# Kernel tuning notes

Hardware: AMD Instinct MI355X
Metric: run time of the kernel (lower is better)

Reference implementation:

```python
import jax, jax.numpy as jnp
import numpy as np

BOS, PAD, EOS, UNK = 0, 1, 2, 3  # fairseq dictionary special-token ids
CHAR_VOCAB = 5000
DIM = 512
LATENT = 10000


def setup_inputs() -> dict:
    key = jax.random.key(0)
    k1, k2, k3 = jax.random.split(key, 3)
    # char-ngram ids per token: [B, T, max_char_len]
    x = jax.random.randint(k1, (8, 1024, 20), 0, CHAR_VOCAB, dtype=jnp.int64 if jax.config.jax_enable_x64 else jnp.int32)
    # char ngram embedding table (also serves as preset_emb for special tokens)
    char_table = jax.random.normal(k2, (CHAR_VOCAB, DIM), dtype=jnp.float32) * 0.05
    # fixed latent codebook, init std = latent**-0.5 as in the module
    latent_mat = jax.random.normal(k3, (LATENT, DIM), dtype=jnp.float32) * (LATENT ** -0.5)
    return {"x": x, "char_table": char_table, "latent_mat": latent_mat}


def reference(x, char_table, latent_mat):
    # --- CharacterNgramEmbedder: gather + sum-pool over char ngrams (pad masked) ---
    emb = char_table[x]                                   # [B, T, C, D]
    valid = (x != PAD)[..., None].astype(emb.dtype)       # pad ngrams contribute 0
    ngram_weight = jnp.sum(emb * valid, axis=2)           # [B, T, D]
    lang_emb = jnp.tanh(ngram_weight)

    # --- latent codebook attention: QK^T -> softmax -> V over fixed codebook ---
    latent_scores = jnp.einsum('btd,ld->btl', lang_emb, latent_mat)   # [B, T, L]
    latent_dist = jax.nn.softmax(latent_scores, axis=-1)
    latent_emb = jnp.einsum('btl,ld->btd', latent_dist, latent_mat)   # [B, T, D]
    sde_emb = lang_emb + latent_emb

    # --- preset_emb overwrite for special tokens (masked scatter) ---
    first = x[:, :, 0]                                    # [B, T]
    for tok in (PAD, BOS, EOS, UNK):
        sde_emb = jnp.where((first == tok)[..., None], char_table[tok], sde_emb)
    return sde_emb
```

## Files before the change

### kernel.cpp

```cpp
#include <hip/hip_runtime.h>

#define BT    8192
#define DIM   512
#define NLAT  10000
#define LPAD2 10240
#define NG    20
#define CV    5000

typedef short bf16x8 __attribute__((ext_vector_type(8)));
typedef float f32x4  __attribute__((ext_vector_type(4)));
typedef unsigned short u16;
typedef u16 u16x8 __attribute__((ext_vector_type(8)));
typedef u16 u16x4 __attribute__((ext_vector_type(4)));

static __device__ __forceinline__ u16 f2bf(float f) {
    union { float f; unsigned u; } v; v.f = f;
    unsigned r = v.u + 0x7FFF + ((v.u >> 16) & 1);
    return (u16)(r >> 16);
}
static __device__ __forceinline__ float bf2f(u16 b) {
    union { unsigned u; float f; } v; v.u = ((unsigned)b) << 16; return v.f;
}

static __device__ __forceinline__ void gload16(const void* g, void* l) {
    __builtin_amdgcn_global_load_lds(
        (const __attribute__((address_space(1))) unsigned int*)g,
        (__attribute__((address_space(3))) unsigned int*)l,
        16, 0, 0);
}

__global__ __launch_bounds__(256) void ct2bf_kernel(
        const float* __restrict__ ct, u16* __restrict__ ctb) {
    const long base = ((long)blockIdx.x * 256 + threadIdx.x) * 8;
    float4 a = *(const float4*)(ct + base);
    float4 b = *(const float4*)(ct + base + 4);
    u16x8 v = { f2bf(a.x), f2bf(a.y), f2bf(a.z), f2bf(a.w),
                f2bf(b.x), f2bf(b.y), f2bf(b.z), f2bf(b.w) };
    *(u16x8*)(ctb + base) = v;
}

__global__ __launch_bounds__(256) void lang_kernel(
        const int* __restrict__ x, const u16* __restrict__ ctb,
        float* __restrict__ lang, u16* __restrict__ qb) {
    const int tok = blockIdx.x * 4 + (threadIdx.x >> 6);
    const int tl  = threadIdx.x & 63;
    const int* xr = x + tok * NG;
    float s[8];
    #pragma unroll
    for (int i = 0; i < 8; ++i) s[i] = 0.f;
    #pragma unroll
    for (int j = 0; j < NG; ++j) {
        int c = xr[j];
        if (c != 1) {
            u16x8 v = *(const u16x8*)(ctb + (long)c * DIM + tl * 8);
            #pragma unroll
            for (int i = 0; i < 8; ++i) s[i] += bf2f(v[i]);
        }
    }
    float4 lo, hi;
    lo.x = tanhf(s[0]); lo.y = tanhf(s[1]); lo.z = tanhf(s[2]); lo.w = tanhf(s[3]);
    hi.x = tanhf(s[4]); hi.y = tanhf(s[5]); hi.z = tanhf(s[6]); hi.w = tanhf(s[7]);
    *(float4*)(lang + (long)tok * DIM + tl * 8)     = lo;
    *(float4*)(lang + (long)tok * DIM + tl * 8 + 4) = hi;
    u16x8 o = { f2bf(lo.x), f2bf(lo.y), f2bf(lo.z), f2bf(lo.w),
                f2bf(hi.x), f2bf(hi.y), f2bf(hi.z), f2bf(hi.w) };
    *(u16x8*)(qb + (long)tok * DIM + tl * 8) = o;
}

__global__ __launch_bounds__(256) void conv_kernel(
        const float* __restrict__ lm, u16* __restrict__ kvg, u16* __restrict__ latT) {
    __shared__ u16 tile[64][514];
    const int lb = blockIdx.x * 64;
    const int t  = threadIdx.x;

    #pragma unroll 4
    for (int i = 0; i < 16; ++i) {
        int ch  = t + i * 256;
        int r   = ch >> 6;
        int c8  = ch & 63;
        int row = lb + r;
        u16x8 v = {0,0,0,0,0,0,0,0};
        if (row < NLAT) {
            const float* src = lm + (long)row * DIM + c8 * 8;
            float4 a = *(const float4*)src;
            float4 b = *(const float4*)(src + 4);
            v[0]=f2bf(a.x); v[1]=f2bf(a.y); v[2]=f2bf(a.z); v[3]=f2bf(a.w);
            v[4]=f2bf(b.x); v[5]=f2bf(b.y); v[6]=f2bf(b.z); v[7]=f2bf(b.w);
        }
        *(u16x8*)(kvg + (long)row * DIM + c8 * 8) = v;
        #pragma unroll
        for (int j = 0; j < 8; ++j) tile[r][c8 * 8 + j] = v[j];
    }
    __syncthreads();
    #pragma unroll 4
    for (int i = 0; i < 16; ++i) {
        int ch = t + i * 256;
        int d  = ch >> 3;
        int c8 = ch & 7;
        u16x8 v;
        #pragma unroll
        for (int j = 0; j < 8; ++j) v[j] = tile[c8 * 8 + j][d];
        *(u16x8*)(latT + (long)d * LPAD2 + lb + c8 * 8) = v;
    }
}

#define G_COMPUTE(buf) {                                                       \
    _Pragma("unroll")                                                          \
    for (int kc_ = 0; kc_ < 2; ++kc_) {                                        \
        const int xs_ = ((kc_ * 4 + g) ^ (lr & 7)) * 8;                        \
        bf16x8 af_[2], bf_[4];                                                 \
        _Pragma("unroll")                                                      \
        for (int mf_ = 0; mf_ < 2; ++mf_)                                      \
            af_[mf_] = *(const bf16x8*)&lds[buf][(wm * 32 + mf_ * 16 + lr) * 64 + xs_]; \
        _Pragma("unroll")                                                      \
        for (int nf_ = 0; nf_ < 4; ++nf_)                                      \
            bf_[nf_] = *(const bf16x8*)&lds[buf][8192 + (wn * 64 + nf_ * 16 + lr) * 64 + xs_]; \
        __builtin_amdgcn_s_setprio(1);                                         \
        _Pragma("unroll")                                                      \
        for (int mf_ = 0; mf_ < 2; ++mf_)                                      \
            _Pragma("unroll")                                                  \
            for (int nf_ = 0; nf_ < 4; ++nf_)                                  \
                acc[mf_][nf_] = __builtin_amdgcn_mfma_f32_16x16x32_bf16(       \
                    af_[mf_], bf_[nf_], acc[mf_][nf_], 0, 0, 0);               \
        __builtin_amdgcn_s_setprio(0);                                         \
    }                                                                          \
}

#define G1_STAGE(buf, kt) {                                                    \
    const int k0_ = (kt) * 64;                                                 \
    _Pragma("unroll")                                                          \
    for (int i_ = 0; i_ < 2; ++i_) {                                           \
        int ch_ = t + i_ * 512;                                                \
        int row_ = ch_ >> 3;                                                   \
        int sc_ = ((ch_ & 7) ^ (row_ & 7)) * 8;                                \
        gload16(Q + (m0 + row_) * (long)DIM + k0_ + sc_, &lds[buf][ch_ * 8]);  \
        gload16(Bgp + (long)row_ * DIM + k0_ + sc_, &lds[buf][8192 + ch_ * 8]);\
    }                                                                          \
}

__global__ __launch_bounds__(512, 4) void gemm1_kernel(
        const u16* __restrict__ Q, const u16* __restrict__ L,
        u16* __restrict__ P, float* __restrict__ rowsum,
        int n0_global, int npanels, int pstride) {
    __shared__ u16 lds[2][16384];

    const int nwg = 64 * npanels;
    const int cpx = nwg >> 3;
    const int bid = blockIdx.x;
    const int wg  = (bid & 7) * cpx + (bid >> 3);
    const int mb  = wg & 63;
    const int nb  = wg >> 6;
    const long m0    = (long)mb * 128;
    const int  ncol0 = n0_global + nb * 128;

    const u16* Bgp = L + (long)ncol0 * DIM;

    const int t = threadIdx.x, lane = t & 63, w = t >> 6;
    const int wm = w >> 1, wn = w & 1;
    const int g = lane >> 4, lr = lane & 15;

    f32x4 acc[2][4];
    #pragma unroll
    for (int m = 0; m < 2; ++m)
        #pragma unroll
        for (int n = 0; n < 4; ++n) acc[m][n] = f32x4{0.f,0.f,0.f,0.f};

    G1_STAGE(0, 0);
    G1_STAGE(1, 1);

    #pragma unroll 1
    for (int kt = 0; kt < 7; ++kt) {
        asm volatile("s_waitcnt vmcnt(4)" ::: "memory");
        __builtin_amdgcn_s_barrier();
        G_COMPUTE(kt & 1);
        __builtin_amdgcn_s_barrier();
        if (kt + 2 < 8) G1_STAGE(kt & 1, kt + 2);
    }
    asm volatile("s_waitcnt vmcnt(0)" ::: "memory");
    __builtin_amdgcn_s_barrier();
    G_COMPUTE(1);

    #pragma unroll
    for (int mf = 0; mf < 2; ++mf)
        #pragma unroll
        for (int nf = 0; nf < 4; ++nf) {
            const int col = ncol0 + wn * 64 + nf * 16 + lr;
            const bool ok = (col < NLAT);
            const int lcol = wn * 64 + nf * 16 + lr;
            #pragma unroll
            for (int r = 0; r < 4; ++r) {
                float p = ok ? __expf(acc[mf][nf][r]) : 0.f;
                acc[mf][nf][r] = p;
                const int row = wm * 32 + mf * 16 + g * 4 + r;
                lds[0][row * 128 + (lcol ^ ((row & 15) << 3))] = f2bf(p);
            }
        }

    #pragma unroll
    for (int mf = 0; mf < 2; ++mf) {
        float sv[4] = {0.f, 0.f, 0.f, 0.f};
        #pragma unroll
        for (int nf = 0; nf < 4; ++nf)
            #pragma unroll
            for (int r = 0; r < 4; ++r) sv[r] += acc[mf][nf][r];
        #pragma unroll
        for (int r = 0; r < 4; ++r) {
            float s = sv[r];
            s += __shfl_xor(s, 1); s += __shfl_xor(s, 2);
            s += __shfl_xor(s, 4); s += __shfl_xor(s, 8);
            if (lr == 0)
                atomicAdd(&rowsum[m0 + wm * 32 + mf * 16 + g * 4 + r], s);
        }
    }

    __syncthreads();
    const int pbase = ncol0 - n0_global;
    #pragma unroll
    for (int it = 0; it < 4; ++it) {
        const int flat = t + it * 512;
        const int row = flat >> 4, ck = flat & 15;
        u16x8 v = *(const u16x8*)&lds[0][row * 128 + ((ck ^ (row & 15)) * 8)];
        *(u16x8*)(P + (m0 + row) * (long)pstride + pbase + ck * 8) = v;
    }
}

#define G2_STAGE(buf, kt) {                                                    \
    const int kloc_ = (step_off + (kt)) * 64;                                  \
    _Pragma("unroll")                                                          \
    for (int i_ = 0; i_ < 2; ++i_) {                                           \
        int ch_ = t + i_ * 512;                                                \
        int row_ = ch_ >> 3;                                                   \
        int sc_ = ((ch_ & 7) ^ (row_ & 7)) * 8;                                \
        gload16(P + (m0 + row_) * (long)pstride + kloc_ + sc_, &lds[buf][ch_ * 8]); \
        gload16(LT + (long)(nbase + row_) * LPAD2 + n0_global + kloc_ + sc_,   \
                &lds[buf][8192 + ch_ * 8]);                                    \
    }                                                                          \
}

__global__ __launch_bounds__(512, 4) void gemm2_kernel(
        const u16* __restrict__ P, const u16* __restrict__ LT,
        float* __restrict__ out, float* __restrict__ part0,
        int pstride, int kcols, int n0_global, int splitk, int accum) {
    __shared__ u16 lds[2][16384];

    const int nwg = 64 * 4 * splitk;
    const int cpx = nwg >> 3;
    const int bid = blockIdx.x;
    const int wg  = (bid & 7) * cpx + (bid >> 3);
    const int mb  = wg & 63;
    const int rest = wg >> 6;
    const int nb  = rest / splitk;
    const int s   = rest % splitk;

    const long m0    = (long)mb * 128;
    const int  nbase = nb * 128;

    const int nsteps = kcols / 64;
    const int q = nsteps / splitk, rr = nsteps % splitk;
    const int psteps   = q + (s < rr ? 1 : 0);
    const int step_off = s * q + (s < rr ? s : rr);

    const int t = threadIdx.x, lane = t & 63, w = t >> 6;
    const int wm = w >> 1, wn = w & 1;
    const int g = lane >> 4, lr = lane & 15;

    float* buf = (s == 0) ? out : part0;

    f32x4 acc[2][4];
    #pragma unroll
    for (int m = 0; m < 2; ++m)
        #pragma unroll
        for (int n = 0; n < 4; ++n) acc[m][n] = f32x4{0.f,0.f,0.f,0.f};

    G2_STAGE(0, 0);
    if (psteps > 1) G2_STAGE(1, 1);

    #pragma unroll 1
    for (int kt = 0; kt < psteps - 1; ++kt) {
        asm volatile("s_waitcnt vmcnt(4)" ::: "memory");
        __builtin_amdgcn_s_barrier();
        G_COMPUTE(kt & 1);
        __builtin_amdgcn_s_barrier();
        if (kt + 2 < psteps) G2_STAGE(kt & 1, kt + 2);
    }
    asm volatile("s_waitcnt vmcnt(0)" ::: "memory");
    __builtin_amdgcn_s_barrier();
    G_COMPUTE((psteps - 1) & 1);

    #pragma unroll
    for (int mf = 0; mf < 2; ++mf)
        #pragma unroll
        for (int nf = 0; nf < 4; ++nf) {
            const int col = nbase + wn * 64 + nf * 16 + lr;
            #pragma unroll
            for (int r = 0; r < 4; ++r) {
                const long row = m0 + wm * 32 + mf * 16 + g * 4 + r;
                float v = acc[mf][nf][r];
                if (accum) v += buf[row * DIM + col];
                buf[row * DIM + col] = v;
            }
        }
}

__global__ __launch_bounds__(256) void final_kernel(
        float* __restrict__ out, const float* __restrict__ part0,
        const float* __restrict__ lang, const float* __restrict__ rowsum,
        const int* __restrict__ x, const float* __restrict__ ct, int nparts) {
    const int tok   = blockIdx.x;
    const float inv = 1.f / rowsum[tok];
    const int first = x[tok * NG];
    #pragma unroll
    for (int i = 0; i < 2; ++i) {
        const int col = threadIdx.x + i * 256;
        float v = out[(long)tok * DIM + col];
        if (nparts > 1) v += part0[(long)tok * DIM + col];
        v = v * inv + lang[(long)tok * DIM + col];
        if (first < 4) v = ct[first * DIM + col];
        out[(long)tok * DIM + col] = v;
    }
}

extern "C" void kernel_launch(void* const* d_in, const int* in_sizes, int n_in,
                              void* d_out, int out_size, void* d_ws, size_t ws_size,
                              hipStream_t stream) {
    const int*   x  = (const int*)d_in[0];
    const float* ct = (const float*)d_in[1];
    const float* lm = (const float*)d_in[2];
    float* out = (float*)d_out;

    char* ws = (char*)d_ws;
    size_t off = 0;
    u16*   qb   = (u16*)(ws + off);   off += (size_t)BT * DIM * 2;
    float* lang = (float*)(ws + off); off += (size_t)BT * DIM * 4;
    u16*   kvg  = (u16*)(ws + off);   off += (size_t)LPAD2 * DIM * 2;
    u16*   latT = (u16*)(ws + off);   off += (size_t)DIM * LPAD2 * 2;
    u16*   ctb  = (u16*)(ws + off);   off += (size_t)CV * DIM * 2;
    float* rowsum = (float*)(ws + off); off += (size_t)BT * 4;
    u16*   P    = (u16*)(ws + off);
    const size_t fixed = off;

    const int panels_total = LPAD2 / 128;
    const size_t pfull = (size_t)BT * LPAD2 * 2;
    const size_t partb = (size_t)BT * DIM * 4;

    int splitk = 1, ppc = panels_total;
    float* part0 = out;
    if (ws_size >= fixed + pfull + partb) {
        splitk = 2;
        part0 = (float*)(ws + fixed + pfull);
    } else if (ws_size >= fixed + pfull) {
        splitk = 1;
    } else {
        size_t avail = (ws_size > fixed) ? (ws_size - fixed) : 0;
        size_t p = avail / ((size_t)BT * 128 * 2);
        ppc = (int)(p < 1 ? 1 : (p > (size_t)panels_total ? (size_t)panels_total : p));
    }
    const int pstride = ppc * 128;

    hipMemsetAsync(rowsum, 0, (size_t)BT * 4, stream);
    ct2bf_kernel<<<CV * DIM / (256 * 8), 256, 0, stream>>>(ct, ctb);
    lang_kernel<<<BT / 4, 256, 0, stream>>>(x, ctb, lang, qb);
    conv_kernel<<<LPAD2 / 64, 256, 0, stream>>>(lm, kvg, latT);

    int chunk = 0;
    for (int cs = 0; cs < panels_total; cs += ppc, ++chunk) {
        const int np = (panels_total - cs < ppc) ? (panels_total - cs) : ppc;
        gemm1_kernel<<<64 * np, 512, 0, stream>>>(qb, kvg, P, rowsum,
                                                  cs * 128, np, pstride);
        gemm2_kernel<<<64 * 4 * splitk, 512, 0, stream>>>(P, latT, out, part0,
                                                          pstride, np * 128, cs * 128,
                                                          splitk, chunk > 0 ? 1 : 0);
    }
    final_kernel<<<BT, 256, 0, stream>>>(out, part0, lang, rowsum, x, ct, splitk);
}
```

Measured before the change: 294.7 us.

## Enlarge gemm1 tile to 256 rows with triple-buffered K=32 pipeline

The QK^T exp kernel now computes 256x128 output tiles per workgroup instead of 128x128, with a 3-stage LDS pipeline over K-steps of 32 and a new swizzle. Rows are grouped into super-tiles when all 80 panels run together, and the lang kernel processes two tokens per wavefront. The aim is better reuse of the latent tile, fewer global loads and more memory-level parallelism in the gather. In exchange the larger accumulator raises register pressure, which may cut occupancy, and the grid shrinks to half as many workgroups.

```diff
diff --git a/kernel.cpp b/kernel.cpp
--- a/kernel.cpp
+++ b/kernel.cpp
@@ -42,29 +42,41 @@
 __global__ __launch_bounds__(256) void lang_kernel(
         const int* __restrict__ x, const u16* __restrict__ ctb,
         float* __restrict__ lang, u16* __restrict__ qb) {
-    const int tok = blockIdx.x * 4 + (threadIdx.x >> 6);
+    const int wv  = threadIdx.x >> 6;
     const int tl  = threadIdx.x & 63;
-    const int* xr = x + tok * NG;
-    float s[8];
-    #pragma unroll
-    for (int i = 0; i < 8; ++i) s[i] = 0.f;
+    const int tok0 = blockIdx.x * 8 + wv * 2;
+    const int* xr0 = x + tok0 * NG;
+    const int* xr1 = xr0 + NG;
+    float s0[8], s1[8];
+    #pragma unroll
+    for (int i = 0; i < 8; ++i) { s0[i] = 0.f; s1[i] = 0.f; }
     #pragma unroll
     for (int j = 0; j < NG; ++j) {
-        int c = xr[j];
-        if (c != 1) {
-            u16x8 v = *(const u16x8*)(ctb + (long)c * DIM + tl * 8);
+        int c0 = xr0[j], c1 = xr1[j];
+        if (c0 != 1) {
+            u16x8 v = *(const u16x8*)(ctb + (long)c0 * DIM + tl * 8);
             #pragma unroll
-            for (int i = 0; i < 8; ++i) s[i] += bf2f(v[i]);
-        }
-    }
-    float4 lo, hi;
-    lo.x = tanhf(s[0]); lo.y = tanhf(s[1]); lo.z = tanhf(s[2]); lo.w = tanhf(s[3]);
-    hi.x = tanhf(s[4]); hi.y = tanhf(s[5]); hi.z = tanhf(s[6]); hi.w = tanhf(s[7]);
-    *(float4*)(lang + (long)tok * DIM + tl * 8)     = lo;
-    *(float4*)(lang + (long)tok * DIM + tl * 8 + 4) = hi;
-    u16x8 o = { f2bf(lo.x), f2bf(lo.y), f2bf(lo.z), f2bf(lo.w),
-                f2bf(hi.x), f2bf(hi.y), f2bf(hi.z), f2bf(hi.w) };
-    *(u16x8*)(qb + (long)tok * DIM + tl * 8) = o;
+            for (int i = 0; i < 8; ++i) s0[i] += bf2f(v[i]);
+        }
+        if (c1 != 1) {
+            u16x8 v = *(const u16x8*)(ctb + (long)c1 * DIM + tl * 8);
+            #pragma unroll
+            for (int i = 0; i < 8; ++i) s1[i] += bf2f(v[i]);
+        }
+    }
+    #pragma unroll
+    for (int p = 0; p < 2; ++p) {
+        float* s = p ? s1 : s0;
+        const long tok = tok0 + p;
+        float4 lo, hi;
+        lo.x = tanhf(s[0]); lo.y = tanhf(s[1]); lo.z = tanhf(s[2]); lo.w = tanhf(s[3]);
+        hi.x = tanhf(s[4]); hi.y = tanhf(s[5]); hi.z = tanhf(s[6]); hi.w = tanhf(s[7]);
+        *(float4*)(lang + tok * DIM + tl * 8)     = lo;
+        *(float4*)(lang + tok * DIM + tl * 8 + 4) = hi;
+        u16x8 o = { f2bf(lo.x), f2bf(lo.y), f2bf(lo.z), f2bf(lo.w),
+                    f2bf(hi.x), f2bf(hi.y), f2bf(hi.z), f2bf(hi.w) };
+        *(u16x8*)(qb + tok * DIM + tl * 8) = o;
+    }
 }
 
 __global__ __launch_bounds__(256) void conv_kernel(
@@ -101,6 +113,153 @@
         #pragma unroll
         for (int j = 0; j < 8; ++j) v[j] = tile[c8 * 8 + j][d];
         *(u16x8*)(latT + (long)d * LPAD2 + lb + c8 * 8) = v;
+    }
+}
+
+#define G1_STAGE(buf, kt) {                                                    \
+    const int k0_ = (kt) * 32;                                                 \
+    {                                                                          \
+        int ch_ = t;                                                           \
+        int row_ = ch_ >> 2, c2_ = ch_ & 3;                                    \
+        int sc_ = (c2_ ^ ((row_ >> 1) & 3)) * 8;                               \
+        gload16(Q + (m0 + row_) * (long)DIM + k0_ + sc_, &lds[buf][ch_ * 8]);  \
+        ch_ = t + 512; row_ = ch_ >> 2; c2_ = ch_ & 3;                         \
+        sc_ = (c2_ ^ ((row_ >> 1) & 3)) * 8;                                   \
+        gload16(Q + (m0 + row_) * (long)DIM + k0_ + sc_, &lds[buf][ch_ * 8]);  \
+        row_ = t >> 2; c2_ = t & 3;                                            \
+        sc_ = (c2_ ^ ((row_ >> 1) & 3)) * 8;                                   \
+        gload16(Bgp + (long)row_ * DIM + k0_ + sc_, &lds[buf][8192 + t * 8]);  \
+    }                                                                          \
+}
+
+#define G1_COMPUTE(buf) {                                                      \
+    bf16x8 af_[4], bf_[4];                                                     \
+    _Pragma("unroll")                                                          \
+    for (int mf_ = 0; mf_ < 4; ++mf_) {                                        \
+        const int rA_ = wm * 64 + mf_ * 16 + lr;                               \
+        const int ck_ = g ^ ((rA_ >> 1) & 3);                                  \
+        af_[mf_] = *(const bf16x8*)&lds[buf][rA_ * 32 + ck_ * 8];              \
+    }                                                                          \
+    _Pragma("unroll")                                                          \
+    for (int nf_ = 0; nf_ < 4; ++nf_) {                                        \
+        const int rB_ = wn * 64 + nf_ * 16 + lr;                               \
+        const int ck_ = g ^ ((rB_ >> 1) & 3);                                  \
+        bf_[nf_] = *(const bf16x8*)&lds[buf][8192 + rB_ * 32 + ck_ * 8];       \
+    }                                                                          \
+    __builtin_amdgcn_s_setprio(1);                                             \
+    _Pragma("unroll")                                                          \
+    for (int mf_ = 0; mf_ < 4; ++mf_)                                          \
+        _Pragma("unroll")                                                      \
+        for (int nf_ = 0; nf_ < 4; ++nf_)                                      \
+            acc[mf_][nf_] = __builtin_amdgcn_mfma_f32_16x16x32_bf16(           \
+                af_[mf_], bf_[nf_], acc[mf_][nf_], 0, 0, 0);                   \
+    __builtin_amdgcn_s_setprio(0);                                             \
+}
+
+#define G1_STEP(kt, vmn) {                                                     \
+    asm volatile("s_waitcnt vmcnt(" #vmn ")" ::: "memory");                    \
+    __builtin_amdgcn_s_barrier();                                              \
+    G1_COMPUTE((kt) % 3);                                                      \
+    __builtin_amdgcn_s_barrier();                                              \
+}
+
+__global__ __launch_bounds__(512, 4) void gemm1_kernel(
+        const u16* __restrict__ Q, const u16* __restrict__ L,
+        u16* __restrict__ P, float* __restrict__ rowsum,
+        int n0_global, int npanels, int pstride) {
+    __shared__ u16 lds[3][12288];
+
+    const int nwg = 32 * npanels;
+    const int cpx = nwg >> 3;
+    const int bid = blockIdx.x;
+    const int wg  = (bid & 7) * cpx + (bid >> 3);
+    int mb, nb;
+    if (npanels == 80) {
+        const int st = wg / 80, lt = wg % 80;
+        const int lmb = lt & 7, lnb = lt >> 3;
+        const int smb = st & 3, snb = st >> 2;
+        mb = smb * 8 + lmb;
+        nb = snb * 10 + lnb;
+    } else {
+        mb = wg & 31;
+        nb = wg >> 5;
+    }
+    const long m0    = (long)mb * 256;
+    const int  ncol0 = n0_global + nb * 128;
+
+    const u16* Bgp = L + (long)ncol0 * DIM;
+
+    const int t = threadIdx.x, lane = t & 63, w = t >> 6;
+    const int wm = w >> 1, wn = w & 1;
+    const int g = lane >> 4, lr = lane & 15;
+
+    f32x4 acc[4][4];
+    #pragma unroll
+    for (int m = 0; m < 4; ++m)
+        #pragma unroll
+        for (int n = 0; n < 4; ++n) acc[m][n] = f32x4{0.f,0.f,0.f,0.f};
+
+    G1_STAGE(0, 0);
+    G1_STAGE(1, 1);
+    G1_STAGE(2, 2);
+
+    #pragma unroll 1
+    for (int kt = 0; kt < 13; ++kt) {
+        asm volatile("s_waitcnt vmcnt(6)" ::: "memory");
+        __builtin_amdgcn_s_barrier();
+        G1_COMPUTE(kt % 3);
+        __builtin_amdgcn_s_barrier();
+        G1_STAGE(kt % 3, kt + 3);
+    }
+    G1_STEP(13, 6);
+    G1_STEP(14, 3);
+    asm volatile("s_waitcnt vmcnt(0)" ::: "memory");
+    __builtin_amdgcn_s_barrier();
+    G1_COMPUTE(15 % 3);
+    __syncthreads();
+
+    u16* lds16 = &lds[0][0];
+    #pragma unroll
+    for (int mf = 0; mf < 4; ++mf)
+        #pragma unroll
+        for (int nf = 0; nf < 4; ++nf) {
+            const int col = ncol0 + wn * 64 + nf * 16 + lr;
+            const bool ok = (col < NLAT);
+            const int lcol = wn * 64 + nf * 16 + lr;
+            #pragma unroll
+            for (int r = 0; r < 4; ++r) {
+                float p = ok ? __expf(acc[mf][nf][r]) : 0.f;
+                acc[mf][nf][r] = p;
+                const int row = wm * 64 + mf * 16 + g * 4 + r;
+                lds16[row * 128 + (lcol ^ ((row & 15) << 3))] = f2bf(p);
+            }
+        }
+
+    #pragma unroll
+    for (int mf = 0; mf < 4; ++mf) {
+        float sv[4] = {0.f, 0.f, 0.f, 0.f};
+        #pragma unroll
+        for (int nf = 0; nf < 4; ++nf)
+            #pragma unroll
+            for (int r = 0; r < 4; ++r) sv[r] += acc[mf][nf][r];
+        #pragma unroll
+        for (int r = 0; r < 4; ++r) {
+            float s = sv[r];
+            s += __shfl_xor(s, 1); s += __shfl_xor(s, 2);
+            s += __shfl_xor(s, 4); s += __shfl_xor(s, 8);
+            if (lr == 0)
+                atomicAdd(&rowsum[m0 + wm * 64 + mf * 16 + g * 4 + r], s);
+        }
+    }
+
+    __syncthreads();
+    const int pbase = ncol0 - n0_global;
+    #pragma unroll
+    for (int it = 0; it < 8; ++it) {
+        const int flat = t + it * 512;
+        const int row = flat >> 4, ck = flat & 15;
+        u16x8 v = *(const u16x8*)&lds16[row * 128 + ((ck ^ (row & 15)) * 8)];
+        *(u16x8*)(P + (m0 + row) * (long)pstride + pbase + ck * 8) = v;
     }
 }
 
@@ -126,104 +285,6 @@
     }                                                                          \
 }
 
-#define G1_STAGE(buf, kt) {                                                    \
-    const int k0_ = (kt) * 64;                                                 \
-    _Pragma("unroll")                                                          \
-    for (int i_ = 0; i_ < 2; ++i_) {                                           \
-        int ch_ = t + i_ * 512;                                                \
-        int row_ = ch_ >> 3;                                                   \
-        int sc_ = ((ch_ & 7) ^ (row_ & 7)) * 8;                                \
-        gload16(Q + (m0 + row_) * (long)DIM + k0_ + sc_, &lds[buf][ch_ * 8]);  \
-        gload16(Bgp + (long)row_ * DIM + k0_ + sc_, &lds[buf][8192 + ch_ * 8]);\
-    }                                                                          \
-}
-
-__global__ __launch_bounds__(512, 4) void gemm1_kernel(
-        const u16* __restrict__ Q, const u16* __restrict__ L,
-        u16* __restrict__ P, float* __restrict__ rowsum,
-        int n0_global, int npanels, int pstride) {
-    __shared__ u16 lds[2][16384];
-
-    const int nwg = 64 * npanels;
-    const int cpx = nwg >> 3;
-    const int bid = blockIdx.x;
-    const int wg  = (bid & 7) * cpx + (bid >> 3);
-    const int mb  = wg & 63;
-    const int nb  = wg >> 6;
-    const long m0    = (long)mb * 128;
-    const int  ncol0 = n0_global + nb * 128;
-
-    const u16* Bgp = L + (long)ncol0 * DIM;
-
-    const int t = threadIdx.x, lane = t & 63, w = t >> 6;
-    const int wm = w >> 1, wn = w & 1;
-    const int g = lane >> 4, lr = lane & 15;
-
-    f32x4 acc[2][4];
-    #pragma unroll
-    for (int m = 0; m < 2; ++m)
-        #pragma unroll
-        for (int n = 0; n < 4; ++n) acc[m][n] = f32x4{0.f,0.f,0.f,0.f};
-
-    G1_STAGE(0, 0);
-    G1_STAGE(1, 1);
-
-    #pragma unroll 1
-    for (int kt = 0; kt < 7; ++kt) {
-        asm volatile("s_waitcnt vmcnt(4)" ::: "memory");
-        __builtin_amdgcn_s_barrier();
-        G_COMPUTE(kt & 1);
-        __builtin_amdgcn_s_barrier();
-        if (kt + 2 < 8) G1_STAGE(kt & 1, kt + 2);
-    }
-    asm volatile("s_waitcnt vmcnt(0)" ::: "memory");
-    __builtin_amdgcn_s_barrier();
-    G_COMPUTE(1);
-
-    #pragma unroll
-    for (int mf = 0; mf < 2; ++mf)
-        #pragma unroll
-        for (int nf = 0; nf < 4; ++nf) {
-            const int col = ncol0 + wn * 64 + nf * 16 + lr;
-            const bool ok = (col < NLAT);
-            const int lcol = wn * 64 + nf * 16 + lr;
-            #pragma unroll
-            for (int r = 0; r < 4; ++r) {
-                float p = ok ? __expf(acc[mf][nf][r]) : 0.f;
-                acc[mf][nf][r] = p;
-                const int row = wm * 32 + mf * 16 + g * 4 + r;
-                lds[0][row * 128 + (lcol ^ ((row & 15) << 3))] = f2bf(p);
-            }
-        }
-
-    #pragma unroll
-    for (int mf = 0; mf < 2; ++mf) {
-        float sv[4] = {0.f, 0.f, 0.f, 0.f};
-        #pragma unroll
-        for (int nf = 0; nf < 4; ++nf)
-            #pragma unroll
-            for (int r = 0; r < 4; ++r) sv[r] += acc[mf][nf][r];
-        #pragma unroll
-        for (int r = 0; r < 4; ++r) {
-            float s = sv[r];
-            s += __shfl_xor(s, 1); s += __shfl_xor(s, 2);
-            s += __shfl_xor(s, 4); s += __shfl_xor(s, 8);
-            if (lr == 0)
-                atomicAdd(&rowsum[m0 + wm * 32 + mf * 16 + g * 4 + r], s);
-        }
-    }
-
-    __syncthreads();
-    const int pbase = ncol0 - n0_global;
-    #pragma unroll
-    for (int it = 0; it < 4; ++it) {
-        const int flat = t + it * 512;
-        const int row = flat >> 4, ck = flat & 15;
-        u16x8 v = *(const u16x8*)&lds[0][row * 128 + ((ck ^ (row & 15)) * 8)];
-        *(u16x8*)(P + (m0 + row) * (long)pstride + pbase + ck * 8) = v;
-    }
-}
-
 #define G2_STAGE(buf, kt) {                                                    \
     const int kloc_ = (step_off + (kt)) * 64;                                  \
     _Pragma("unroll")                                                          \
@@ -354,18 +415,19 @@
         size_t avail = (ws_size > fixed) ? (ws_size - fixed) : 0;
         size_t p = avail / ((size_t)BT * 128 * 2);
         ppc = (int)(p < 1 ? 1 : (p > (size_t)panels_total ? (size_t)panels_total : p));
+        if (ppc & 1) ppc = (ppc > 1) ? ppc - 1 : 1;
     }
     const int pstride = ppc * 128;
 
     hipMemsetAsync(rowsum, 0, (size_t)BT * 4, stream);
     ct2bf_kernel<<<CV * DIM / (256 * 8), 256, 0, stream>>>(ct, ctb);
-    lang_kernel<<<BT / 4, 256, 0, stream>>>(x, ctb, lang, qb);
+    lang_kernel<<<BT / 8, 256, 0, stream>>>(x, ctb, lang, qb);
     conv_kernel<<<LPAD2 / 64, 256, 0, stream>>>(lm, kvg, latT);
 
     int chunk = 0;
     for (int cs = 0; cs < panels_total; cs += ppc, ++chunk) {
         const int np = (panels_total - cs < ppc) ? (panels_total - cs) : ppc;
-        gemm1_kernel<<<64 * np, 512, 0, stream>>>(qb, kvg, P, rowsum,
+        gemm1_kernel<<<32 * np, 512, 0, stream>>>(qb, kvg, P, rowsum,
                                                   cs * 128, np, pstride);
         gemm2_kernel<<<64 * 4 * splitk, 512, 0, stream>>>(P, latT, out, part0,
                                                           pstride, np * 128, cs * 128,
```

Measured after the change: 286.2 us. 1.03x faster.
